# Performance work log

Hardware: AMD Instinct MI355X
Metric: run time of the kernel (lower is better)

The kernel has to match this reference:

```python
import jax, jax.numpy as jnp
import numpy as np

N = 32          # num_vars
H = 128         # encoder_hidden
HR = 128        # encoder_rnn_hidden
NE = 2          # num_edge_types
INP = 4         # input_size
B, T = 4, 50


def _xavier(k, shape):
    # torch Linear weight is [out, in]; xavier_normal_ std
    fan_out, fan_in = shape
    std = (2.0 / (fan_in + fan_out)) ** 0.5
    return jax.random.normal(k, shape, jnp.float32) * std


def setup_inputs() -> dict:
    key = jax.random.key(0)
    ks = jax.random.split(key, 24)
    pairs = np.array([[i, j] for i in range(N) for j in range(N) if i != j], dtype=np.int32).T
    b = lambda n: jnp.full((n,), 0.1, jnp.float32)  # bias init 0.1 per init_weights
    return {
        "inputs": jax.random.normal(ks[0], (B, T, N, INP), jnp.float32),
        "edge_index": jnp.asarray(pairs),                       # [2, E]
        # node embedding MLP (MLPEncoder_SingleTime): inp->H (ELU) ->H
        "W_ne1": _xavier(ks[1], (H, INP)), "b_ne1": b(H),
        "W_ne2": _xavier(ks[2], (H, H)),   "b_ne2": b(H),
        # EdgeConv nn: Linear(2H -> H), aggr='max'
        "W_ec": _xavier(ks[3], (H, 2 * H)), "b_ec": b(H),
        # edge_self_encoder: Linear(1->2H), ELU, Linear(2H->H)
        "W_es1": _xavier(ks[4], (2 * H, 1)),   "b_es1": b(2 * H),
        "W_es2": _xavier(ks[5], (H, 2 * H)),   "b_es2": b(H),
        # forward GRU
        "Wih_f": _xavier(ks[6], (3 * HR, H)),  "Whh_f": _xavier(ks[7], (3 * HR, HR)),
        "bih_f": b(3 * HR), "bhh_f": b(3 * HR),
        # reverse GRU
        "Wih_r": _xavier(ks[8], (3 * HR, H)),  "Whh_r": _xavier(ks[9], (3 * HR, HR)),
        "bih_r": b(3 * HR), "bhh_r": b(3 * HR),
        # heads (num_layers == 1 -> single Linear)
        "W_pf": _xavier(ks[10], (NE, HR)),     "b_pf": b(NE),
        "W_ef": _xavier(ks[11], (NE, 2 * HR)), "b_ef": b(NE),
    }


def _gru(seq, Wih, Whh, bih, bhh):
    # seq: [S, T, H] batch_first; torch GRU equations, h0 = 0
    gx = jnp.moveaxis(seq @ Wih.T + bih, 1, 0)  # [T, S, 3HR]

    def step(h, gxt):
        gh = h @ Whh.T + bhh
        xr, xz, xn = jnp.split(gxt, 3, -1)
        hr, hz, hn = jnp.split(gh, 3, -1)
        r = jax.nn.sigmoid(xr + hr)
        z = jax.nn.sigmoid(xz + hz)
        n = jnp.tanh(xn + r * hn)
        h_new = (1.0 - z) * n + z * h
        return h_new, h_new

    h0 = jnp.zeros((seq.shape[0], Whh.shape[1]), seq.dtype)
    h_last, outs = jax.lax.scan(step, h0, gx)
    return jnp.moveaxis(outs, 0, 1), h_last  # [S,T,HR], [S,HR]


def reference(inputs, edge_index, W_ne1, b_ne1, W_ne2, b_ne2, W_ec, b_ec,
              W_es1, b_es1, W_es2, b_es2, Wih_f, Whh_f, bih_f, bhh_f,
              Wih_r, Whh_r, bih_r, bhh_r, W_pf, b_pf, W_ef, b_ef):
    src, dst = edge_index[0], edge_index[1]
    E = src.shape[0]

    x = jnp.transpose(inputs, (0, 2, 1, 3))            # [B, N, T, INP]
    ne = jax.nn.elu(x @ W_ne1.T + b_ne1) @ W_ne2.T + b_ne2  # [B, N, T, H]

    # EdgeConv (max aggr): msg = Lin(cat(x_i, x_j - x_i)), i=target(dst), j=source(src)
    x_i = ne[:, dst]                                   # [B, E, T, H]
    x_j = ne[:, src]
    msg = jnp.concatenate([x_i, x_j - x_i], -1) @ W_ec.T + b_ec   # [B, E, T, H]
    agg = jax.ops.segment_max(jnp.moveaxis(msg, 1, 0), dst, num_segments=N)  # [N,B,T,H]
    node_embeddings = jnp.moveaxis(agg, 0, 1)          # [B, N, T, H]

    # edge_self_attention: scaled dot of node pair -> MLP(1 -> 2H -> H)
    dots = jnp.sum(node_embeddings[:, src] * node_embeddings[:, dst], -1) / H  # [B,E,T]
    ef = jax.nn.elu(dots[..., None] @ W_es1.T + b_es1) @ W_es2.T + b_es2       # [B,E,T,H]

    seq = ef.reshape(-1, ef.shape[2], H)               # [B*E, T, H]
    fwd_x, h_last = _gru(seq, Wih_f, Whh_f, bih_f, bhh_f)
    rev_x, _ = _gru(seq[:, ::-1], Wih_r, Whh_r, bih_r, bhh_r)
    rev_x = rev_x[:, ::-1]
    prior_state = h_last[None]                          # [1, B*E, HR]

    Bsz = ef.shape[0]
    prior_result = (fwd_x @ W_pf.T + b_pf).reshape(Bsz, E, -1, NE).transpose(0, 2, 1, 3)
    combined = jnp.concatenate([fwd_x, rev_x], -1)
    encoder_result = (combined @ W_ef.T + b_ef).reshape(Bsz, E, -1, NE).transpose(0, 2, 1, 3)
    return prior_result, encoder_result, prior_state, node_embeddings
```

## Files before the change

kernel.cpp:

```cpp
#include <hip/hip_runtime.h>
#include <hip/hip_bf16.h>

typedef unsigned int u32;
typedef unsigned short u16;
typedef short bf16x8 __attribute__((ext_vector_type(8)));
typedef float f32x4  __attribute__((ext_vector_type(4)));

#define O0 0
#define O1 396800
#define O2 793600
#define O3 1301504

#define AOF_INP   0
#define AOF_WNE1  25600
#define AOF_BNE1  26112
#define AOF_WNE2  26240
#define AOF_BNE2  42624
#define AOF_WEC   42752
#define AOF_BEC   75520
#define AOF_WES1  75648
#define AOF_BES1  75904
#define AOF_WES2  76160
#define AOF_BES2  108928
#define AOF_WIHF  109056
#define AOF_WHHF  158208
#define AOF_BIHF  207360
#define AOF_BHHF  207744
#define AOF_WIHR  208128
#define AOF_WHHR  257280
#define AOF_BIHR  306432
#define AOF_BHHR  306816
#define AOF_WPF   307200
#define AOF_BPF   307456
#define AOF_WEF   307464
#define AOF_BEF   307976

__device__ __forceinline__ float bf2f(u16 v){ return __uint_as_float(((u32)v)<<16); }
__device__ __forceinline__ u16 f2b(float x){ __hip_bfloat16 h = __float2bfloat16(x); return *reinterpret_cast<u16*>(&h); }
#if __has_builtin(__builtin_amdgcn_rcpf)
__device__ __forceinline__ float frcp(float x){ return __builtin_amdgcn_rcpf(x); }
#else
__device__ __forceinline__ float frcp(float x){ return 1.f/x; }
#endif
__device__ __forceinline__ float sigmf(float x){ return frcp(1.f + __expf(-x)); }
__device__ __forceinline__ float tanhfast(float x){ return 1.f - 2.f*frcp(__expf(2.f*x)+1.f); }
__device__ __forceinline__ float eluf(float x){ return x>0.f ? x : __expf(x)-1.f; }
__device__ __forceinline__ void store_out(void* out, int idx, float v, int isbf){
  if (isbf) ((u16*)out)[idx] = f2b(v); else ((float*)out)[idx] = v;
}

struct P23 { const void* p[23]; };
struct S23 { int n[23]; };

__global__ __launch_bounds__(256) void k_cvt(P23 ps, S23 sz, u16* __restrict__ arena,
                                             u16* __restrict__ Wuv, int* __restrict__ flag)
{
  static const int offs[23] = {0,25600,26112,26240,42624,42752,75520,75648,75904,76160,
                               108928,109056,158208,207360,207744,208128,257280,306432,
                               306816,307200,307456,307464,307976};
  int sgi = blockIdx.x;
  u32 w0 = *(const u32*)ps.p[2];
  int isbf = ((w0 >> 16) == (w0 & 0xffffu));
  if (sgi == 0 && threadIdx.x == 0) *flag = isbf;
  if (sgi < 23){
    const void* src = ps.p[sgi];
    int off = offs[sgi], n = sz.n[sgi];
    if (isbf){
      const u16* s16 = (const u16*)src;
      for (int i = threadIdx.x; i < n; i += 256) arena[off+i] = s16[i];
    } else {
      const float* s32 = (const float*)src;
      for (int i = threadIdx.x; i < n; i += 256) arena[off+i] = f2b(s32[i]);
    }
  } else {
    if (isbf){
      const u16* wec = (const u16*)ps.p[5];
      for (int i = threadIdx.x; i < 32768; i += 256){
        int r = i>>7, k = i&127;
        float vv = (r<128) ? (bf2f(wec[r*256+k]) - bf2f(wec[r*256+128+k]))
                           : bf2f(wec[(r-128)*256+128+k]);
        Wuv[i] = f2b(vv);
      }
    } else {
      const float* wec = (const float*)ps.p[5];
      for (int i = threadIdx.x; i < 32768; i += 256){
        int r = i>>7, k = i&127;
        float vv = (r<128) ? (wec[r*256+k] - wec[r*256+128+k])
                           : wec[(r-128)*256+128+k];
        Wuv[i] = f2b(vv);
      }
    }
  }
}

__global__ __launch_bounds__(256) void k_uvgram(
    const u16* __restrict__ arena, const u16* __restrict__ Wuv,
    float* __restrict__ g, void* __restrict__ out, const int* __restrict__ flag)
{
  const int bt = blockIdx.x; const int b = bt/50, t = bt%50;
  const int tid = threadIdx.x;
  const int l = tid & 63, col = l & 15, lk = l >> 4, wv = tid >> 6;
  const int isbf = *flag;

  __shared__ char ldsb[54784];
  u16*   h1b = (u16*)(ldsb);
  u16*   neb = (u16*)(ldsb + 8704);
  float* uf  = (float*)(ldsb + 17408);
  float* vf  = (float*)(ldsb + 34304);
  float* m1s = (float*)(ldsb + 51200);
  float* m2s = (float*)(ldsb + 52224);
  int*   ams = (int*)  (ldsb + 53248);
  float* Af  = (float*)(ldsb);
  float* xL  = (float*)(ldsb + 54272);

  if (tid < 128) xL[tid] = bf2f(arena[AOF_INP + bt*128 + tid]);
  __syncthreads();
  #pragma unroll
  for (int it=0; it<16; ++it){
    int i = tid + it*256; int n = i>>7, j = i&127;
    const u16* w1 = arena + AOF_WNE1 + j*4;
    float a = bf2f(arena[AOF_BNE1+j]) + bf2f(w1[0])*xL[n*4] + bf2f(w1[1])*xL[n*4+1]
            + bf2f(w1[2])*xL[n*4+2] + bf2f(w1[3])*xL[n*4+3];
    h1b[n*128 + (j ^ ((n&7)*8))] = f2b(eluf(a));
  }
  __syncthreads();
  {
    const int sw = (col&7)*8, k8 = lk*8;
    #pragma unroll
    for (int jt=0; jt<2; ++jt){
      int j = wv*32 + jt*16 + col;
      bf16x8 b0 = *(const bf16x8*)(arena + AOF_WNE2 + j*128 +  0 + k8);
      bf16x8 b1 = *(const bf16x8*)(arena + AOF_WNE2 + j*128 + 32 + k8);
      bf16x8 b2 = *(const bf16x8*)(arena + AOF_WNE2 + j*128 + 64 + k8);
      bf16x8 b3 = *(const bf16x8*)(arena + AOF_WNE2 + j*128 + 96 + k8);
      float bj = bf2f(arena[AOF_BNE2 + j]);
      f32x4 a0 = f32x4{bj,bj,bj,bj}, a1 = f32x4{bj,bj,bj,bj};
      a0 = __builtin_amdgcn_mfma_f32_16x16x32_bf16(*(const bf16x8*)&h1b[col*128 + (( 0+k8)^sw)], b0, a0, 0,0,0);
      a0 = __builtin_amdgcn_mfma_f32_16x16x32_bf16(*(const bf16x8*)&h1b[col*128 + ((32+k8)^sw)], b1, a0, 0,0,0);
      a0 = __builtin_amdgcn_mfma_f32_16x16x32_bf16(*(const bf16x8*)&h1b[col*128 + ((64+k8)^sw)], b2, a0, 0,0,0);
      a0 = __builtin_amdgcn_mfma_f32_16x16x32_bf16(*(const bf16x8*)&h1b[col*128 + ((96+k8)^sw)], b3, a0, 0,0,0);
      a1 = __builtin_amdgcn_mfma_f32_16x16x32_bf16(*(const bf16x8*)&h1b[(16+col)*128 + (( 0+k8)^sw)], b0, a1, 0,0,0);
      a1 = __builtin_amdgcn_mfma_f32_16x16x32_bf16(*(const bf16x8*)&h1b[(16+col)*128 + ((32+k8)^sw)], b1, a1, 0,0,0);
      a1 = __builtin_amdgcn_mfma_f32_16x16x32_bf16(*(const bf16x8*)&h1b[(16+col)*128 + ((64+k8)^sw)], b2, a1, 0,0,0);
      a1 = __builtin_amdgcn_mfma_f32_16x16x32_bf16(*(const bf16x8*)&h1b[(16+col)*128 + ((96+k8)^sw)], b3, a1, 0,0,0);
      #pragma unroll
      for (int r4=0;r4<4;++r4){
        int r0 = lk*4+r4;
        neb[r0*128      + (j ^ ((r0&7)*8))] = f2b(a0[r4]);
        neb[(16+r0)*128 + (j ^ ((r0&7)*8))] = f2b(a1[r4]);
      }
    }
  }
  __syncthreads();
  {
    const int sw = (col&7)*8, k8 = lk*8;
    #pragma unroll
    for (int jt=0; jt<4; ++jt){
      int rbase = wv*64 + jt*16;
      int r = rbase + col;
      bf16x8 b0 = *(const bf16x8*)(Wuv + r*128 +  0 + k8);
      bf16x8 b1 = *(const bf16x8*)(Wuv + r*128 + 32 + k8);
      bf16x8 b2 = *(const bf16x8*)(Wuv + r*128 + 64 + k8);
      bf16x8 b3 = *(const bf16x8*)(Wuv + r*128 + 96 + k8);
      f32x4 a0 = f32x4{0.f,0.f,0.f,0.f}, a1 = f32x4{0.f,0.f,0.f,0.f};
      a0 = __builtin_amdgcn_mfma_f32_16x16x32_bf16(*(const bf16x8*)&neb[col*128 + (( 0+k8)^sw)], b0, a0, 0,0,0);
      a0 = __builtin_amdgcn_mfma_f32_16x16x32_bf16(*(const bf16x8*)&neb[col*128 + ((32+k8)^sw)], b1, a0, 0,0,0);
      a0 = __builtin_amdgcn_mfma_f32_16x16x32_bf16(*(const bf16x8*)&neb[col*128 + ((64+k8)^sw)], b2, a0, 0,0,0);
      a0 = __builtin_amdgcn_mfma_f32_16x16x32_bf16(*(const bf16x8*)&neb[col*128 + ((96+k8)^sw)], b3, a0, 0,0,0);
      a1 = __builtin_amdgcn_mfma_f32_16x16x32_bf16(*(const bf16x8*)&neb[(16+col)*128 + (( 0+k8)^sw)], b0, a1, 0,0,0);
      a1 = __builtin_amdgcn_mfma_f32_16x16x32_bf16(*(const bf16x8*)&neb[(16+col)*128 + ((32+k8)^sw)], b1, a1, 0,0,0);
      a1 = __builtin_amdgcn_mfma_f32_16x16x32_bf16(*(const bf16x8*)&neb[(16+col)*128 + ((64+k8)^sw)], b2, a1, 0,0,0);
      a1 = __builtin_amdgcn_mfma_f32_16x16x32_bf16(*(const bf16x8*)&neb[(16+col)*128 + ((96+k8)^sw)], b3, a1, 0,0,0);
      float* dst = (rbase < 128) ? uf : vf;
      int cc = (rbase < 128) ? r : (r-128);
      #pragma unroll
      for (int r4=0;r4<4;++r4){
        dst[(lk*4+r4)*132 + cc]    = a0[r4];
        dst[(16+lk*4+r4)*132 + cc] = a1[r4];
      }
    }
  }
  __syncthreads();
  int half = tid >> 7, h = tid & 127;
  {
    float m1=-1e30f, m2=-1e30f; int am=-1;
    int s0 = half*16;
    #pragma unroll
    for (int s=s0; s<s0+16; ++s){
      float v = vf[s*132+h];
      if (v>m1){ m2=m1; m1=v; am=s; } else if (v>m2) m2=v;
    }
    m1s[half*128+h]=m1; m2s[half*128+h]=m2; ams[half*128+h]=am;
  }
  __syncthreads();
  if (tid < 128){
    float m1a=m1s[h], m1b=m1s[128+h], m2a=m2s[h], m2b=m2s[128+h];
    int ama=ams[h], amb=ams[128+h];
    float M1, M2; int AM;
    if (m1a >= m1b){ M1=m1a; AM=ama; M2=fmaxf(m2a, m1b); }
    else           { M1=m1b; AM=amb; M2=fmaxf(m1a, m2b); }
    m1s[h]=M1; m2s[h]=M2; ams[h]=AM;
  }
  __syncthreads();
  #pragma unroll
  for (int it=0; it<16; ++it){
    int i = tid + it*256; int d=i>>7, k=i&127;
    float val = uf[d*132+k] + bf2f(arena[AOF_BEC+k]) + ((d==ams[k]) ? m2s[k] : m1s[k]);
    Af[d*133+k] = val;
    store_out(out, O3 + ((b*32+d)*50+t)*128+k, val, isbf);
  }
  __syncthreads();
  #pragma unroll
  for (int pp=0; pp<4; ++pp){
    int p = tid + pp*256; int s=p>>5, d=p&31;
    float acc=0.f;
    #pragma unroll 8
    for (int k=0;k<128;++k) acc += Af[s*133+k]*Af[d*133+k];
    if (s != d){
      int e = s*31 + d - (d>s ? 1 : 0);
      g[(b*992 + e)*50 + t] = acc * (1.f/128.f);
    }
  }
}

__global__ __launch_bounds__(256) void k_ef(
    const u16* __restrict__ arena, const float* __restrict__ g, u16* __restrict__ ef)
{
  const int c0 = blockIdx.x * 64;
  const int tid = threadIdx.x;
  __shared__ u16 zb[64][256];
  __shared__ u16 ob[64][128];
  {
    int r = tid >> 2, cg = (tid & 3) * 64;
    int rs = (r&7)*8;
    float gv = g[c0 + r];
    #pragma unroll
    for (int q=0;q<8;++q){
      int cc = cg + q*8;
      u32 w0,w1,w2,w3;
      { float z0=eluf(bf2f(arena[AOF_WES1+cc  ])*gv+bf2f(arena[AOF_BES1+cc  ]));
        float z1=eluf(bf2f(arena[AOF_WES1+cc+1])*gv+bf2f(arena[AOF_BES1+cc+1]));
        w0=(u32)f2b(z0)|((u32)f2b(z1)<<16); }
      { float z0=eluf(bf2f(arena[AOF_WES1+cc+2])*gv+bf2f(arena[AOF_BES1+cc+2]));
        float z1=eluf(bf2f(arena[AOF_WES1+cc+3])*gv+bf2f(arena[AOF_BES1+cc+3]));
        w1=(u32)f2b(z0)|((u32)f2b(z1)<<16); }
      { float z0=eluf(bf2f(arena[AOF_WES1+cc+4])*gv+bf2f(arena[AOF_BES1+cc+4]));
        float z1=eluf(bf2f(arena[AOF_WES1+cc+5])*gv+bf2f(arena[AOF_BES1+cc+5]));
        w2=(u32)f2b(z0)|((u32)f2b(z1)<<16); }
      { float z0=eluf(bf2f(arena[AOF_WES1+cc+6])*gv+bf2f(arena[AOF_BES1+cc+6]));
        float z1=eluf(bf2f(arena[AOF_WES1+cc+7])*gv+bf2f(arena[AOF_BES1+cc+7]));
        w3=(u32)f2b(z0)|((u32)f2b(z1)<<16); }
      *(uint4*)&zb[r][cc ^ rs] = uint4{w0,w1,w2,w3};
    }
  }
  __syncthreads();
  const int l = tid & 63, col = l & 15, lk = l >> 4, wv = tid >> 6;
  const int sw = (col&7)*8, k8 = lk*8;
  #pragma unroll
  for (int nt2=0; nt2<2; ++nt2){
    int jt = (wv*2+nt2)*16;
    bf16x8 bfr[8];
    #pragma unroll
    for (int ks=0;ks<8;++ks) bfr[ks] = *(const bf16x8*)(arena + AOF_WES2 + (jt+col)*256 + ks*32 + k8);
    int j0 = jt + lk*4;
    f32x4 binit = f32x4{ bf2f(arena[AOF_BES2+j0]), bf2f(arena[AOF_BES2+j0+1]),
                         bf2f(arena[AOF_BES2+j0+2]), bf2f(arena[AOF_BES2+j0+3]) };
    #pragma unroll
    for (int mt=0; mt<4; ++mt){
      f32x4 a = binit;
      #pragma unroll
      for (int ks=0;ks<8;++ks)
        a = __builtin_amdgcn_mfma_f32_16x16x32_bf16(bfr[ks], *(const bf16x8*)&zb[16*mt+col][(ks*32 + k8) ^ sw], a, 0,0,0);
      u32 lo = (u32)f2b(a[0]) | ((u32)f2b(a[1])<<16);
      u32 hi = (u32)f2b(a[2]) | ((u32)f2b(a[3])<<16);
      *(uint2*)&ob[16*mt+col][j0 ^ ((col&7)*8)] = uint2{lo,hi};
    }
  }
  __syncthreads();
  #pragma unroll
  for (int i4 = tid; i4 < 1024; i4 += 256){
    int row = i4 >> 4, seg = i4 & 15;
    uint4 v = *(const uint4*)&ob[row][(seg*8) ^ ((row&7)*8)];
    *(uint4*)&ef[(c0 + row)*128 + seg*8] = v;
  }
}

__global__ __launch_bounds__(512, 2) void k_gru2(
    const u16* __restrict__ arena, const u16* __restrict__ ef,
    float* __restrict__ encA, float* __restrict__ encB,
    void* __restrict__ out, const int* __restrict__ flag)
{
  const int dir = blockIdx.y;
  const int tid = threadIdx.x;
  const int w   = tid >> 6;
  const int l   = tid & 63;
  const int col = l & 15;
  const int lk  = l >> 4;
  const int seq0 = blockIdx.x * 32;
  const int isbf = *flag;

  const u16* Whh = arena + (dir ? AOF_WHHR : AOF_WHHF);
  const u16* Wih = arena + (dir ? AOF_WIHR : AOF_WIHF);
  const int  bhoff = dir ? AOF_BHHR : AOF_BHHF;
  const int  bioff = dir ? AOF_BIHR : AOF_BIHF;

  bf16x8 wbx[3][4], wbh[3][4], pwf[4];
  #pragma unroll
  for (int j=0;j<3;++j){
    int gate = j*128 + 16*w + col;
    #pragma unroll
    for (int ks=0;ks<4;++ks){
      wbx[j][ks] = *(const bf16x8*)(Wih + gate*128 + ks*32 + lk*8);
      wbh[j][ks] = *(const bf16x8*)(Whh + gate*128 + ks*32 + lk*8);
    }
  }
  #pragma unroll
  for (int ks=0;ks<4;++ks){
    bf16x8 v = bf16x8{0,0,0,0,0,0,0,0};
    int k0 = ks*32 + lk*8;
    if (col < 4){
      if (dir==0) v = (col<2) ? *(const bf16x8*)(arena + AOF_WPF + col*128 + k0)
                              : *(const bf16x8*)(arena + AOF_WEF + (col-2)*256 + k0);
      else if (col>=2) v = *(const bf16x8*)(arena + AOF_WEF + (col-2)*256 + 128 + k0);
    }
    pwf[ks] = v;
  }
  const float bias_r  = bf2f(arena[bioff       + 16*w + col]) + bf2f(arena[bhoff       + 16*w + col]);
  const float bias_z  = bf2f(arena[bioff + 128 + 16*w + col]) + bf2f(arena[bhoff + 128 + 16*w + col]);
  const float bias_xn = bf2f(arena[bioff + 256 + 16*w + col]);
  const float bias_hn = bf2f(arena[bhoff + 256 + 16*w + col]);
  const float bpc = (col==1) ? bf2f(arena[AOF_BPF+1]) : bf2f(arena[AOF_BPF]);

  int eb0, eb1, eb2v, eb3;
  { int sq0b = seq0 + (w==1 ? 16 : 0) + lk*4;
    int b0=(sq0b  )/992, b1=(sq0b+1)/992, b2=(sq0b+2)/992, b3=(sq0b+3)/992;
    eb0 = b0*99200 + (sq0b   - b0*992)*2;
    eb1 = b1*99200 + (sq0b+1 - b1*992)*2;
    eb2v= b2*99200 + (sq0b+2 - b2*992)*2;
    eb3 = b3*99200 + (sq0b+3 - b3*992)*2; }

  __shared__ u16 efb[2][32][128];
  __shared__ u16 hbuf[2][32][128];
  const u16* efp = ef + (seq0 + (tid>>4))*6400 + (tid&15)*8;
  const int ldr = tid>>4;
  const int ldsw = ((tid&15)*8) ^ ((ldr&7)*8);

  for (int i=tid; i<4096; i+=512) ((u16*)hbuf[0])[i] = 0;
  { int t0 = dir ? 49 : 0;
    uint4 s0 = *(const uint4*)(efp + t0*128);
    *(uint4*)&efb[0][ldr][ldsw] = s0; }
  uint4 stgB;
  { int t1 = dir ? 48 : 1;
    stgB = *(const uint4*)(efp + t1*128); }
  __syncthreads();

#define PROJ_STORE(H0,H1,H2,H3, TP) do { \
    f32x4 ap = f32x4{0.f,0.f,0.f,0.f}; \
    ap = __builtin_amdgcn_mfma_f32_16x16x32_bf16(H0, pwf[0], ap, 0,0,0); \
    ap = __builtin_amdgcn_mfma_f32_16x16x32_bf16(H1, pwf[1], ap, 0,0,0); \
    ap = __builtin_amdgcn_mfma_f32_16x16x32_bf16(H2, pwf[2], ap, 0,0,0); \
    ap = __builtin_amdgcn_mfma_f32_16x16x32_bf16(H3, pwf[3], ap, 0,0,0); \
    if (col < 4){ \
      int tof = (TP)*1984; \
      if (dir == 0){ \
        if (col < 2){ \
          store_out(out, O0 + eb0  + tof + col, ap[0] + bpc, isbf); \
          store_out(out, O0 + eb1  + tof + col, ap[1] + bpc, isbf); \
          store_out(out, O0 + eb2v + tof + col, ap[2] + bpc, isbf); \
          store_out(out, O0 + eb3  + tof + col, ap[3] + bpc, isbf); \
        } else { \
          encA[eb0  + tof + col-2] = ap[0]; \
          encA[eb1  + tof + col-2] = ap[1]; \
          encA[eb2v + tof + col-2] = ap[2]; \
          encA[eb3  + tof + col-2] = ap[3]; \
        } \
      } else if (col >= 2){ \
        encB[eb0  + tof + col-2] = ap[0]; \
        encB[eb1  + tof + col-2] = ap[1]; \
        encB[eb2v + tof + col-2] = ap[2]; \
        encB[eb3  + tof + col-2] = ap[3]; \
      } \
    } \
  } while(0)

#define STEP_MT2(MT, HO, P, IT) do { \
    const int sw_ = (col&7)*8, k8_ = lk*8; \
    bf16x8 hf0 = *(const bf16x8*)&hbuf[P][16*(MT)+col][(( 0+k8_)^sw_)]; \
    bf16x8 hf1 = *(const bf16x8*)&hbuf[P][16*(MT)+col][((32+k8_)^sw_)]; \
    bf16x8 hf2 = *(const bf16x8*)&hbuf[P][16*(MT)+col][((64+k8_)^sw_)]; \
    bf16x8 hf3 = *(const bf16x8*)&hbuf[P][16*(MT)+col][((96+k8_)^sw_)]; \
    if (w == (MT) && (IT) > 0){ \
      int tp = dir ? (50-(IT)) : ((IT)-1); \
      PROJ_STORE(hf0,hf1,hf2,hf3, tp); \
    } \
    f32x4 ar  = f32x4{bias_r,bias_r,bias_r,bias_r}; \
    f32x4 az  = f32x4{bias_z,bias_z,bias_z,bias_z}; \
    f32x4 axn = f32x4{bias_xn,bias_xn,bias_xn,bias_xn}; \
    f32x4 ahn = f32x4{bias_hn,bias_hn,bias_hn,bias_hn}; \
    _Pragma("unroll") \
    for (int ks=0;ks<4;++ks){ \
      bf16x8 a = *(const bf16x8*)&efb[P][16*(MT)+col][((ks*32 + k8_)^sw_)]; \
      ar  = __builtin_amdgcn_mfma_f32_16x16x32_bf16(a, wbx[0][ks], ar,  0,0,0); \
      az  = __builtin_amdgcn_mfma_f32_16x16x32_bf16(a, wbx[1][ks], az,  0,0,0); \
      axn = __builtin_amdgcn_mfma_f32_16x16x32_bf16(a, wbx[2][ks], axn, 0,0,0); \
    } \
    ar  = __builtin_amdgcn_mfma_f32_16x16x32_bf16(hf0, wbh[0][0], ar,  0,0,0); \
    az  = __builtin_amdgcn_mfma_f32_16x16x32_bf16(hf0, wbh[1][0], az,  0,0,0); \
    ahn = __builtin_amdgcn_mfma_f32_16x16x32_bf16(hf0, wbh[2][0], ahn, 0,0,0); \
    ar  = __builtin_amdgcn_mfma_f32_16x16x32_bf16(hf1, wbh[0][1], ar,  0,0,0); \
    az  = __builtin_amdgcn_mfma_f32_16x16x32_bf16(hf1, wbh[1][1], az,  0,0,0); \
    ahn = __builtin_amdgcn_mfma_f32_16x16x32_bf16(hf1, wbh[2][1], ahn, 0,0,0); \
    ar  = __builtin_amdgcn_mfma_f32_16x16x32_bf16(hf2, wbh[0][2], ar,  0,0,0); \
    az  = __builtin_amdgcn_mfma_f32_16x16x32_bf16(hf2, wbh[1][2], az,  0,0,0); \
    ahn = __builtin_amdgcn_mfma_f32_16x16x32_bf16(hf2, wbh[2][2], ahn, 0,0,0); \
    ar  = __builtin_amdgcn_mfma_f32_16x16x32_bf16(hf3, wbh[0][3], ar,  0,0,0); \
    az  = __builtin_amdgcn_mfma_f32_16x16x32_bf16(hf3, wbh[1][3], az,  0,0,0); \
    ahn = __builtin_amdgcn_mfma_f32_16x16x32_bf16(hf3, wbh[2][3], ahn, 0,0,0); \
    _Pragma("unroll") \
    for (int r4=0;r4<4;++r4){ \
      float rr = sigmf(ar[r4]); \
      float zz = sigmf(az[r4]); \
      float nn = tanhfast(axn[r4] + rr*ahn[r4]); \
      (HO)[r4] = (1.f-zz)*nn + zz*(HO)[r4]; \
      hbuf[1-(P)][16*(MT)+lk*4+r4][(16*w+col) ^ (((lk*4+r4)&7)*8)] = f2b((HO)[r4]); \
    } \
  } while(0)

  f32x4 ho0 = f32x4{0.f,0.f,0.f,0.f};
  f32x4 ho1 = f32x4{0.f,0.f,0.f,0.f};

  for (int k2=0; k2<25; ++k2){
    const int it0 = 2*k2, it1 = 2*k2+1;
    uint4 stgA;
    { int tn = dir ? (49-(it0+2)) : (it0+2);
      tn = tn < 0 ? 0 : (tn > 49 ? 49 : tn);
      stgA = *(const uint4*)(efp + tn*128); }
    STEP_MT2(0, ho0, 0, it0);
    STEP_MT2(1, ho1, 0, it0);
    *(uint4*)&efb[1][ldr][ldsw] = stgB;
    __syncthreads();
    { int tn = dir ? (49-(it1+2)) : (it1+2);
      tn = tn < 0 ? 0 : (tn > 49 ? 49 : tn);
      stgB = *(const uint4*)(efp + tn*128); }
    STEP_MT2(0, ho0, 1, it1);
    STEP_MT2(1, ho1, 1, it1);
    *(uint4*)&efb[0][ldr][ldsw] = stgA;
    __syncthreads();
  }

  if (w < 2){
    const int sw_ = (col&7)*8, k8_ = lk*8;
    bf16x8 hf0 = *(const bf16x8*)&hbuf[0][16*w+col][(( 0+k8_)^sw_)];
    bf16x8 hf1 = *(const bf16x8*)&hbuf[0][16*w+col][((32+k8_)^sw_)];
    bf16x8 hf2 = *(const bf16x8*)&hbuf[0][16*w+col][((64+k8_)^sw_)];
    bf16x8 hf3 = *(const bf16x8*)&hbuf[0][16*w+col][((96+k8_)^sw_)];
    int tp = dir ? 0 : 49;
    PROJ_STORE(hf0,hf1,hf2,hf3, tp);
  }
  if (dir == 0){
    for (int i=tid; i<4096; i+=512){
      int s=i>>7, k=i&127;
      store_out(out, O2 + (seq0+s)*128 + k, bf2f(hbuf[0][s][k ^ ((s&7)*8)]), isbf);
    }
  }
#undef STEP_MT2
#undef PROJ_STORE
}

__global__ __launch_bounds__(256) void k_comb(
    const float* __restrict__ encA, const float* __restrict__ encB,
    const u16* __restrict__ arena, void* __restrict__ out, const int* __restrict__ flag)
{
  int i = (blockIdx.x*256 + threadIdx.x)*2;
  float2 a = *(const float2*)&encA[i];
  float2 c = *(const float2*)&encB[i];
  float e0 = a.x + c.x + bf2f(arena[AOF_BEF]);
  float e1 = a.y + c.y + bf2f(arena[AOF_BEF+1]);
  if (*flag){
    u32 pk = (u32)f2b(e0) | ((u32)f2b(e1)<<16);
    ((u32*)out)[(O1>>1) + blockIdx.x*256 + threadIdx.x] = pk;
  } else {
    ((float*)out)[O1+i] = e0;
    ((float*)out)[O1+i+1] = e1;
  }
}

extern "C" void kernel_launch(void* const* d_in, const int* in_sizes, int n_in,
                              void* d_out, int out_size, void* d_ws, size_t ws_size,
                              hipStream_t stream)
{
  P23 ps; S23 sz;
  ps.p[0] = d_in[0]; sz.n[0] = in_sizes[0];
  for (int k=1;k<23;++k){ ps.p[k] = d_in[k+1]; sz.n[k] = in_sizes[k+1]; }

  char* ws = (char*)d_ws;
  u16*   arena = (u16*)  (ws);
  int*   flag  = (int*)  (ws +   616064);
  u16*   Wuv   = (u16*)  (ws +  1012480);
  float* g     = (float*)(ws +  1078016);
  float* encA  = (float*)(ws +  1871616);
  float* encB  = (float*)(ws +  3458816);
  u16*   ef    = (u16*)  (ws +  5046016);

  k_cvt    <<<dim3(24),     dim3(256), 0, stream>>>(ps, sz, arena, Wuv, flag);
  k_uvgram <<<dim3(200),    dim3(256), 0, stream>>>(arena, Wuv, g, d_out, flag);
  k_ef     <<<dim3(3100),   dim3(256), 0, stream>>>(arena, g, ef);
  k_gru2   <<<dim3(124, 2), dim3(512), 0, stream>>>(arena, ef, encA, encB, d_out, flag);
  k_comb   <<<dim3(775),    dim3(256), 0, stream>>>(encA, encB, arena, d_out, flag);
}
```

Baseline: 198.9 us.

## Fuse edge-feature MLP into the uv-gram kernel and drop the g buffer

```diff
diff --git a/kernel.cpp b/kernel.cpp
--- a/kernel.cpp
+++ b/kernel.cpp
@@ -95,7 +95,7 @@
 
 __global__ __launch_bounds__(256) void k_uvgram(
     const u16* __restrict__ arena, const u16* __restrict__ Wuv,
-    float* __restrict__ g, void* __restrict__ out, const int* __restrict__ flag)
+    u16* __restrict__ ef, void* __restrict__ out, const int* __restrict__ flag)
 {
   const int bt = blockIdx.x; const int b = bt/50, t = bt%50;
   const int tid = threadIdx.x;
@@ -112,6 +112,9 @@
   int*   ams = (int*)  (ldsb + 53248);
   float* Af  = (float*)(ldsb);
   float* xL  = (float*)(ldsb + 54272);
+  float* dv  = (float*)(ldsb + 49152);
+  u16*   zb  = (u16*)(ldsb);
+  u16*   ob  = (u16*)(ldsb + 32768);
 
   if (tid < 128) xL[tid] = bf2f(arena[AOF_INP + bt*128 + tid]);
   __syncthreads();
@@ -216,72 +219,80 @@
     float acc=0.f;
     #pragma unroll 8
     for (int k=0;k<128;++k) acc += Af[s*133+k]*Af[d*133+k];
-    if (s != d){
-      int e = s*31 + d - (d>s ? 1 : 0);
-      g[(b*992 + e)*50 + t] = acc * (1.f/128.f);
-    }
-  }
-}
-
-__global__ __launch_bounds__(256) void k_ef(
-    const u16* __restrict__ arena, const float* __restrict__ g, u16* __restrict__ ef)
-{
-  const int c0 = blockIdx.x * 64;
-  const int tid = threadIdx.x;
-  __shared__ u16 zb[64][256];
-  __shared__ u16 ob[64][128];
+    dv[p] = acc * (1.f/128.f);
+  }
+  __syncthreads();
+  bf16x8 wes2f[2][8]; f32x4 binit2[2];
   {
-    int r = tid >> 2, cg = (tid & 3) * 64;
-    int rs = (r&7)*8;
-    float gv = g[c0 + r];
+    const int k8 = lk*8;
     #pragma unroll
-    for (int q=0;q<8;++q){
-      int cc = cg + q*8;
-      u32 w0,w1,w2,w3;
-      { float z0=eluf(bf2f(arena[AOF_WES1+cc  ])*gv+bf2f(arena[AOF_BES1+cc  ]));
-        float z1=eluf(bf2f(arena[AOF_WES1+cc+1])*gv+bf2f(arena[AOF_BES1+cc+1]));
-        w0=(u32)f2b(z0)|((u32)f2b(z1)<<16); }
-      { float z0=eluf(bf2f(arena[AOF_WES1+cc+2])*gv+bf2f(arena[AOF_BES1+cc+2]));
-        float z1=eluf(bf2f(arena[AOF_WES1+cc+3])*gv+bf2f(arena[AOF_BES1+cc+3]));
-        w1=(u32)f2b(z0)|((u32)f2b(z1)<<16); }
-      { float z0=eluf(bf2f(arena[AOF_WES1+cc+4])*gv+bf2f(arena[AOF_BES1+cc+4]));
-        float z1=eluf(bf2f(arena[AOF_WES1+cc+5])*gv+bf2f(arena[AOF_BES1+cc+5]));
-        w2=(u32)f2b(z0)|((u32)f2b(z1)<<16); }
-      { float z0=eluf(bf2f(arena[AOF_WES1+cc+6])*gv+bf2f(arena[AOF_BES1+cc+6]));
-        float z1=eluf(bf2f(arena[AOF_WES1+cc+7])*gv+bf2f(arena[AOF_BES1+cc+7]));
-        w3=(u32)f2b(z0)|((u32)f2b(z1)<<16); }
-      *(uint4*)&zb[r][cc ^ rs] = uint4{w0,w1,w2,w3};
-    }
-  }
-  __syncthreads();
-  const int l = tid & 63, col = l & 15, lk = l >> 4, wv = tid >> 6;
-  const int sw = (col&7)*8, k8 = lk*8;
-  #pragma unroll
-  for (int nt2=0; nt2<2; ++nt2){
-    int jt = (wv*2+nt2)*16;
-    bf16x8 bfr[8];
-    #pragma unroll
-    for (int ks=0;ks<8;++ks) bfr[ks] = *(const bf16x8*)(arena + AOF_WES2 + (jt+col)*256 + ks*32 + k8);
-    int j0 = jt + lk*4;
-    f32x4 binit = f32x4{ bf2f(arena[AOF_BES2+j0]), bf2f(arena[AOF_BES2+j0+1]),
-                         bf2f(arena[AOF_BES2+j0+2]), bf2f(arena[AOF_BES2+j0+3]) };
-    #pragma unroll
-    for (int mt=0; mt<4; ++mt){
-      f32x4 a = binit;
+    for (int nt2=0; nt2<2; ++nt2){
+      int jt = (wv*2+nt2)*16;
       #pragma unroll
       for (int ks=0;ks<8;++ks)
-        a = __builtin_amdgcn_mfma_f32_16x16x32_bf16(bfr[ks], *(const bf16x8*)&zb[16*mt+col][(ks*32 + k8) ^ sw], a, 0,0,0);
-      u32 lo = (u32)f2b(a[0]) | ((u32)f2b(a[1])<<16);
-      u32 hi = (u32)f2b(a[2]) | ((u32)f2b(a[3])<<16);
-      *(uint2*)&ob[16*mt+col][j0 ^ ((col&7)*8)] = uint2{lo,hi};
-    }
-  }
-  __syncthreads();
-  #pragma unroll
-  for (int i4 = tid; i4 < 1024; i4 += 256){
-    int row = i4 >> 4, seg = i4 & 15;
-    uint4 v = *(const uint4*)&ob[row][(seg*8) ^ ((row&7)*8)];
-    *(uint4*)&ef[(c0 + row)*128 + seg*8] = v;
+        wes2f[nt2][ks] = *(const bf16x8*)(arena + AOF_WES2 + (jt+col)*256 + ks*32 + k8);
+      int j0 = jt + lk*4;
+      binit2[nt2] = f32x4{ bf2f(arena[AOF_BES2+j0]), bf2f(arena[AOF_BES2+j0+1]),
+                           bf2f(arena[AOF_BES2+j0+2]), bf2f(arena[AOF_BES2+j0+3]) };
+    }
+  }
+  const int sw2 = (col&7)*8, k82 = lk*8;
+  for (int c=0; c<16; ++c){
+    const int nrows = (c==15) ? 32 : 64;
+    {
+      int r = tid >> 2, cg = (tid & 3) * 64;
+      if (r < nrows){
+        int e = c*64 + r;
+        int s = e/31, r31 = e - s*31;
+        int d = r31 + (r31 >= s ? 1 : 0);
+        float gv = dv[s*32+d];
+        int rs = (r&7)*8;
+        #pragma unroll
+        for (int q=0;q<8;++q){
+          int cc = cg + q*8;
+          u32 w0,w1,w2,w3;
+          { float z0=eluf(bf2f(arena[AOF_WES1+cc  ])*gv+bf2f(arena[AOF_BES1+cc  ]));
+            float z1=eluf(bf2f(arena[AOF_WES1+cc+1])*gv+bf2f(arena[AOF_BES1+cc+1]));
+            w0=(u32)f2b(z0)|((u32)f2b(z1)<<16); }
+          { float z0=eluf(bf2f(arena[AOF_WES1+cc+2])*gv+bf2f(arena[AOF_BES1+cc+2]));
+            float z1=eluf(bf2f(arena[AOF_WES1+cc+3])*gv+bf2f(arena[AOF_BES1+cc+3]));
+            w1=(u32)f2b(z0)|((u32)f2b(z1)<<16); }
+          { float z0=eluf(bf2f(arena[AOF_WES1+cc+4])*gv+bf2f(arena[AOF_BES1+cc+4]));
+            float z1=eluf(bf2f(arena[AOF_WES1+cc+5])*gv+bf2f(arena[AOF_BES1+cc+5]));
+            w2=(u32)f2b(z0)|((u32)f2b(z1)<<16); }
+          { float z0=eluf(bf2f(arena[AOF_WES1+cc+6])*gv+bf2f(arena[AOF_BES1+cc+6]));
+            float z1=eluf(bf2f(arena[AOF_WES1+cc+7])*gv+bf2f(arena[AOF_BES1+cc+7]));
+            w3=(u32)f2b(z0)|((u32)f2b(z1)<<16); }
+          *(uint4*)&zb[r*256 + (cc ^ rs)] = uint4{w0,w1,w2,w3};
+        }
+      }
+    }
+    __syncthreads();
+    #pragma unroll
+    for (int nt2=0; nt2<2; ++nt2){
+      int j0 = (wv*2+nt2)*16 + lk*4;
+      #pragma unroll
+      for (int mt=0; mt<4; ++mt){
+        if (16*mt < nrows){
+          f32x4 a = binit2[nt2];
+          #pragma unroll
+          for (int ks=0;ks<8;++ks)
+            a = __builtin_amdgcn_mfma_f32_16x16x32_bf16(wes2f[nt2][ks],
+                  *(const bf16x8*)&zb[(16*mt+col)*256 + ((ks*32 + k82) ^ sw2)], a, 0,0,0);
+          u32 lo = (u32)f2b(a[0]) | ((u32)f2b(a[1])<<16);
+          u32 hi = (u32)f2b(a[2]) | ((u32)f2b(a[3])<<16);
+          *(uint2*)&ob[(16*mt+col)*128 + (j0 ^ ((col&7)*8))] = uint2{lo,hi};
+        }
+      }
+    }
+    __syncthreads();
+    for (int i4 = tid; i4 < nrows*16; i4 += 256){
+      int row = i4 >> 4, seg = i4 & 15;
+      uint4 v = *(const uint4*)&ob[row*128 + ((seg*8) ^ ((row&7)*8))];
+      int e = c*64 + row;
+      *(uint4*)&ef[(b*992 + e)*6400 + t*128 + seg*8] = v;
+    }
+    __syncthreads();
   }
 }
 
@@ -497,14 +508,12 @@
   u16*   arena = (u16*)  (ws);
   int*   flag  = (int*)  (ws +   616064);
   u16*   Wuv   = (u16*)  (ws +  1012480);
-  float* g     = (float*)(ws +  1078016);
   float* encA  = (float*)(ws +  1871616);
   float* encB  = (float*)(ws +  3458816);
   u16*   ef    = (u16*)  (ws +  5046016);
 
   k_cvt    <<<dim3(24),     dim3(256), 0, stream>>>(ps, sz, arena, Wuv, flag);
-  k_uvgram <<<dim3(200),    dim3(256), 0, stream>>>(arena, Wuv, g, d_out, flag);
-  k_ef     <<<dim3(3100),   dim3(256), 0, stream>>>(arena, g, ef);
+  k_uvgram <<<dim3(200),    dim3(256), 0, stream>>>(arena, Wuv, ef, d_out, flag);
   k_gru2   <<<dim3(124, 2), dim3(512), 0, stream>>>(arena, ef, encA, encB, d_out, flag);
   k_comb   <<<dim3(775),    dim3(256), 0, stream>>>(encA, encB, arena, d_out, flag);
 }
```

After: 199.2 us. No clear change (+0.2%).
